# Optimization experiments

Measured on AMD Instinct MI355X. Metric: run time of the kernel, lower is better.

Reference implementation:

```python
import jax, jax.numpy as jnp
import numpy as np

THRESH = 0.5
IOU_THR = 0.3
TOP_K = 512

# standard YOLOv3 anchors for strides 32/16/8 (grids 13/26/52)
ANCHORS_13 = jnp.array([[116., 90.], [156., 198.], [373., 326.]], dtype=jnp.float32)
ANCHORS_26 = jnp.array([[30., 61.], [62., 45.], [59., 119.]], dtype=jnp.float32)
ANCHORS_52 = jnp.array([[10., 13.], [16., 30.], [33., 23.]], dtype=jnp.float32)


def _decode(out, stride, anchors):
    # out: [B, 3*(5+C), H, W] -> [B, H, W, 3, 5+C] (matches permute(0,2,3,1).reshape)
    B, _, H, W = out.shape
    o = jnp.transpose(out, (0, 2, 3, 1)).reshape(B, H, W, 3, -1)
    conf = jax.nn.sigmoid(o[..., 4])          # [B,H,W,3]
    xy = jax.nn.sigmoid(o[..., 0:2])          # sigmoid on x,y as in _filter
    gy = jnp.arange(H, dtype=o.dtype)[None, :, None, None]   # idxs[:,1]
    gx = jnp.arange(W, dtype=o.dtype)[None, None, :, None]   # idxs[:,2]
    cy = (gy + xy[..., 1]) * stride
    cx = (gx + xy[..., 0]) * stride
    w = anchors[:, 0] * jnp.exp(o[..., 2])    # anchors broadcast over anchor dim
    h = anchors[:, 1] * jnp.exp(o[..., 3])
    cls = jnp.argmax(o[..., 5:], axis=-1).astype(o.dtype)
    n = jnp.broadcast_to(jnp.arange(B, dtype=o.dtype)[:, None, None, None], conf.shape)
    w0, h0 = w * 0.5, h * 0.5
    boxes = jnp.stack([conf, cx - w0, cy - h0, cx + w0, cy + h0, cls, n], axis=-1)
    return boxes.reshape(-1, 7), conf.reshape(-1)


def _iou_matrix(b):
    # b: [K,4] = x1,y1,x2,y2 -> [K,K] IoU
    area = jnp.clip(b[:, 2] - b[:, 0], 0) * jnp.clip(b[:, 3] - b[:, 1], 0)
    xx1 = jnp.maximum(b[:, None, 0], b[None, :, 0])
    yy1 = jnp.maximum(b[:, None, 1], b[None, :, 1])
    xx2 = jnp.minimum(b[:, None, 2], b[None, :, 2])
    yy2 = jnp.minimum(b[:, None, 3], b[None, :, 3])
    inter = jnp.clip(xx2 - xx1, 0) * jnp.clip(yy2 - yy1, 0)
    return inter / (area[:, None] + area[None, :] - inter + 1e-9)


def _detect(output_13, output_26, output_52):
    b13, c13 = _decode(output_13, 32.0, ANCHORS_13)
    b26, c26 = _decode(output_26, 16.0, ANCHORS_26)
    b52, c52 = _decode(output_52, 8.0, ANCHORS_52)
    boxes = jnp.concatenate([b13, b26, b52], axis=0)      # [N,7]
    conf = jnp.concatenate([c13, c26, c52], axis=0)       # [N]
    # threshold filter (mask instead of nonzero-compaction for fixed shapes)
    scores = jnp.where(conf > THRESH, conf, 0.0)
    top_scores, idx = jax.lax.top_k(scores, TOP_K)        # sorted descending
    cand = boxes[idx]                                      # [K,7]
    valid = top_scores > THRESH
    iou = _iou_matrix(cand[:, 1:5])
    ar = jnp.arange(TOP_K)

    def body(i, keep):
        sup = keep[i] & (iou[i] > IOU_THR) & (ar > i)
        return keep & ~sup

    keep = jax.lax.fori_loop(0, TOP_K, body, valid)
    # zero out suppressed / invalid rows; rows: [conf, x1, y1, x2, y2, cls, batch]
    return cand * keep[:, None].astype(cand.dtype)


def setup_inputs() -> dict:
    key = jax.random.key(0)
    k1, k2, k3 = jax.random.split(key, 3)
    return {
        "output_13": jax.random.normal(k1, (32, 255, 13, 13), dtype=jnp.float32),
        "output_26": jax.random.normal(k2, (32, 255, 26, 26), dtype=jnp.float32),
        "output_52": jax.random.normal(k3, (32, 255, 52, 52), dtype=jnp.float32),
    }


def reference(output_13, output_26, output_52):
    return _detect(output_13, output_26, output_52)
```

## Files before the change

kernel.cpp:

```cpp
#include <hip/hip_runtime.h>

#define N13E 16224
#define N26E 64896
#define NTOT 340704
#define BASE26 16224
#define BASE52 81120
#define KMAX 2048
#define TOPK 512

__device__ __forceinline__ float sigm(float x) { return 1.0f / (1.0f + expf(-x)); }

__device__ __forceinline__ unsigned long long pack_key(float v, int c) {
    unsigned u = __float_as_uint(v);
    unsigned ov = (u & 0x80000000u) ? ~u : (u | 0x80000000u);
    return (((unsigned long long)ov) << 32) | (unsigned long long)(unsigned)(127 - c);
}

template <int HW>
__device__ __forceinline__ float load_logit(const float* __restrict__ p, int local) {
    int ba = local / HW;
    int hw = local - ba * HW;
    int b = ba / 3;
    int a = ba - b * 3;
    return p[(b * 255 + a * 85 + 4) * HW + hw];
}

__global__ void __launch_bounds__(256) k_hist(const float* __restrict__ p13,
                                              const float* __restrict__ p26,
                                              const float* __restrict__ p52,
                                              unsigned* __restrict__ hist) {
    int t = blockIdx.x * 256 + threadIdx.x;
    if (t >= NTOT) return;
    float logit;
    if (t < N13E)               logit = load_logit<169>(p13, t);
    else if (t < N13E + N26E)   logit = load_logit<676>(p26, t - N13E);
    else                        logit = load_logit<2704>(p52, t - (N13E + N26E));
    float conf = sigm(logit);
    if (conf > 0.5f) {
        unsigned bin = (__float_as_uint(conf) >> 12) - 0x3F000u;
        bin = (bin > 2047u) ? 2047u : bin;
        atomicAdd(&hist[bin], 1u);
    }
}

template <int HW, int BASE>
__device__ __forceinline__ void compact_one(const float* __restrict__ p, int local, unsigned thrv,
                                            unsigned* __restrict__ cnt,
                                            unsigned long long* __restrict__ keys) {
    int ba = local / HW;
    int hw = local - ba * HW;
    int b = ba / 3;
    int a = ba - b * 3;
    float logit = p[(b * 255 + a * 85 + 4) * HW + hw];
    float conf = sigm(logit);
    unsigned bits = __float_as_uint(conf);
    if (conf > 0.5f && bits >= thrv) {
        unsigned pos = atomicAdd(cnt, 1u);
        if (pos < (unsigned)KMAX) {
            unsigned concat = (unsigned)(BASE + (b * HW + hw) * 3 + a);
            keys[pos] = (((unsigned long long)bits) << 32) | (unsigned long long)(0xFFFFFFFFu - concat);
        }
    }
}

__global__ void __launch_bounds__(512) k_compact_scan(const float* __restrict__ p13,
                                                      const float* __restrict__ p26,
                                                      const float* __restrict__ p52,
                                                      const unsigned* __restrict__ hist,
                                                      unsigned* __restrict__ cnt,
                                                      unsigned long long* __restrict__ keys) {
    __shared__ unsigned tot[512];
    __shared__ unsigned thrS;
    int tid = threadIdx.x;

    unsigned loc[4]; unsigned s = 0u;
#pragma unroll
    for (int k = 0; k < 4; ++k) { loc[k] = hist[2047 - (tid * 4 + k)]; s += loc[k]; }
    tot[tid] = s;
    __syncthreads();
    for (int off = 1; off < 512; off <<= 1) {
        unsigned u = (tid >= off) ? tot[tid - off] : 0u;
        __syncthreads();
        tot[tid] += u;
        __syncthreads();
    }
    unsigned excl = tot[tid] - s;
    unsigned total = tot[511];
    if (total < (unsigned)TOPK) {
        if (tid == 0) thrS = 0x3F000001u;
    } else {
        unsigned run = excl;
#pragma unroll
        for (int k = 0; k < 4; ++k) {
            unsigned c = run + loc[k];
            if (run < (unsigned)TOPK && c >= (unsigned)TOPK) {
                int bin = 2047 - (tid * 4 + k);
                thrS = ((unsigned)(bin + 0x3F000)) << 12;
            }
            run = c;
        }
    }
    __syncthreads();
    unsigned thrv = thrS;

    int t = blockIdx.x * 512 + tid;
    if (t >= NTOT) return;
    if (t < N13E)               compact_one<169, 0>(p13, t, thrv, cnt, keys);
    else if (t < N13E + N26E)   compact_one<676, BASE26>(p26, t - N13E, thrv, cnt, keys);
    else                        compact_one<2704, BASE52>(p52, t - (N13E + N26E), thrv, cnt, keys);
}

template <int HW, int W>
__device__ __forceinline__ void decode64(const float* __restrict__ p, int local, float strideF,
                                         float aw0, float ah0, float aw1, float ah1, float aw2, float ah2,
                                         float conf, float* __restrict__ outrow, int lane) {
    int a = local % 3;
    int cell = local / 3;
    int b = cell / HW;
    int hw = cell - b * HW;
    int h = hw / W;
    int wc = hw - h * W;
    int cb = b * 255 + a * 85;
    float v1 = p[(cb + 5 + lane) * HW + hw];
    unsigned long long k1 = pack_key(v1, lane);
    if (lane < 16) {
        float v2 = p[(cb + 69 + lane) * HW + hw];
        unsigned long long k2 = pack_key(v2, lane + 64);
        if (k2 > k1) k1 = k2;
    }
#pragma unroll
    for (int m = 32; m >= 1; m >>= 1) {
        unsigned long long o = __shfl_xor(k1, m, 64);
        if (o > k1) k1 = o;
    }
    if (lane == 0) {
        int cls = 127 - (int)(unsigned)(k1 & 0xFFFFFFFFull);
        float t0 = p[(cb + 0) * HW + hw];
        float t1 = p[(cb + 1) * HW + hw];
        float t2 = p[(cb + 2) * HW + hw];
        float t3 = p[(cb + 3) * HW + hw];
        float aw = (a == 0) ? aw0 : ((a == 1) ? aw1 : aw2);
        float ah = (a == 0) ? ah0 : ((a == 1) ? ah1 : ah2);
        float sx = sigm(t0);
        float sy = sigm(t1);
        float bw = aw * expf(t2);
        float bh = ah * expf(t3);
        float cx = ((float)wc + sx) * strideF;
        float cy = ((float)h + sy) * strideF;
        float w0 = bw * 0.5f, h0 = bh * 0.5f;
        outrow[0] = conf;
        outrow[1] = cx - w0;
        outrow[2] = cy - h0;
        outrow[3] = cx + w0;
        outrow[4] = cy + h0;
        outrow[5] = (float)cls;
        outrow[6] = (float)b;
    }
}

__global__ void __launch_bounds__(512) k_rank_decode(const float* __restrict__ p13,
                                                     const float* __restrict__ p26,
                                                     const float* __restrict__ p52,
                                                     const unsigned* __restrict__ cnt,
                                                     const unsigned long long* __restrict__ keys,
                                                     float* __restrict__ cand) {
    __shared__ unsigned long long keysL[KMAX];
    __shared__ unsigned long long sortedL[8];
    int tid = threadIdx.x;

    unsigned n = *cnt; if (n > (unsigned)KMAX) n = (unsigned)KMAX;
    int npad = ((int)n + 7) & ~7;
    for (int j = tid; j < npad; j += 512) keysL[j] = (j < (int)n) ? keys[j] : 0ull;
    if (tid < 8) sortedL[tid] = 0ull;
    __syncthreads();
    int lo = blockIdx.x * 8;
    unsigned long long mine[4]; unsigned rk[4]; int nown = 0;
#pragma unroll
    for (int k = 0; k < 4; ++k) {
        int idx = tid + k * 512;
        if (idx < (int)n) { mine[nown] = keysL[idx]; rk[nown] = 0u; ++nown; }
    }
    for (int j = 0; j < npad; j += 8) {
        unsigned long long kk[8];
#pragma unroll
        for (int u = 0; u < 8; ++u) kk[u] = keysL[j + u];
        for (int m = 0; m < nown; ++m) {
            unsigned acc = 0u;
#pragma unroll
            for (int u = 0; u < 8; ++u) acc += (kk[u] > mine[m]) ? 1u : 0u;
            rk[m] += acc;
        }
    }
    for (int m = 0; m < nown; ++m) {
        unsigned r = rk[m];
        if (r >= (unsigned)lo && r < (unsigned)(lo + 8)) sortedL[r - lo] = mine[m];
    }
    __syncthreads();

    int bb = tid >> 6;
    int lane = tid & 63;
    int box = lo + bb;
    unsigned long long key = sortedL[bb];
    unsigned sb = (unsigned)(key >> 32);
    float* row = cand + box * 7;
    if (sb == 0u) {
        if (lane < 7) row[lane] = 0.0f;
        return;
    }
    unsigned idx = 0xFFFFFFFFu - (unsigned)(key & 0xFFFFFFFFull);
    float conf = __uint_as_float(sb);
    if (idx < N13E)
        decode64<169, 13>(p13, (int)idx, 32.0f, 116.f, 90.f, 156.f, 198.f, 373.f, 326.f, conf, row, lane);
    else if (idx < N13E + N26E)
        decode64<676, 26>(p26, (int)idx - BASE26, 16.0f, 30.f, 61.f, 62.f, 45.f, 59.f, 119.f, conf, row, lane);
    else
        decode64<2704, 52>(p52, (int)idx - BASE52, 8.0f, 10.f, 13.f, 16.f, 30.f, 33.f, 23.f, conf, row, lane);
}

__global__ void __launch_bounds__(512) k_mask(const float* __restrict__ cand,
                                              unsigned long long* __restrict__ smaskG) {
    __shared__ float sx1[TOPK], sy1[TOPK], sx2[TOPK], sy2[TOPK];
    int tid = threadIdx.x;
    for (int p = tid; p < TOPK; p += 512) {
        const float* r = cand + p * 7;
        sx1[p] = r[1]; sy1[p] = r[2]; sx2[p] = r[3]; sy2[p] = r[4];
    }
    __syncthreads();
    int wv = tid >> 6;
    int lane = tid & 63;
    int gwave = blockIdx.x * 8 + wv;
#pragma unroll
    for (int q = 0; q < 16; ++q) {
        int word = gwave * 16 + q;
        int i = word >> 3, jw = word & 7;
        int j = jw * 64 + lane;
        float ix1 = sx1[i], iy1 = sy1[i], ix2 = sx2[i], iy2 = sy2[i];
        float ai = fmaxf(ix2 - ix1, 0.f) * fmaxf(iy2 - iy1, 0.f);
        float jx1 = sx1[j], jy1 = sy1[j], jx2 = sx2[j], jy2 = sy2[j];
        float aj = fmaxf(jx2 - jx1, 0.f) * fmaxf(jy2 - jy1, 0.f);
        float xx1 = fmaxf(ix1, jx1), yy1 = fmaxf(iy1, jy1);
        float xx2 = fminf(ix2, jx2), yy2 = fminf(iy2, jy2);
        float inter = fmaxf(xx2 - xx1, 0.f) * fmaxf(yy2 - yy1, 0.f);
        float iou = inter / (((ai + aj) - inter) + 1e-9f);
        bool bit = (j > i) && (iou > 0.3f);
        unsigned long long m = __ballot(bit);
        if (lane == 0) smaskG[word] = m;
    }
}

__global__ void __launch_bounds__(512) k_sweep(const float* __restrict__ cand,
                                               const unsigned long long* __restrict__ smaskG,
                                               float* __restrict__ out) {
    __shared__ unsigned long long smask[TOPK * 8];
    __shared__ unsigned long long live[8], keepw[8];
    int tid = threadIdx.x;
    for (int p = tid; p < TOPK * 8; p += 512) smask[p] = smaskG[p];
    bool validt = cand[tid * 7] > 0.5f;
    unsigned long long bal = __ballot(validt);
    if ((tid & 63) == 0) live[tid >> 6] = bal;
    __syncthreads();
    if (tid < 64) {
        int lane = tid;
        int lw = lane & 7;
        unsigned long long r = 0ull;
#pragma unroll
        for (int w = 0; w < 8; ++w) {
            unsigned long long lvw = live[w];
#pragma unroll 8
            for (int b2 = 0; b2 < 64; ++b2) {
                int i = w * 64 + b2;
                unsigned long long rowv = smask[i * 8 + lw];
                unsigned rlo = (unsigned)__builtin_amdgcn_readlane((int)(unsigned)(r & 0xFFFFFFFFull), w);
                unsigned rhi = (unsigned)__builtin_amdgcn_readlane((int)(unsigned)(r >> 32), w);
                unsigned long long rw = (((unsigned long long)rhi) << 32) | (unsigned long long)rlo;
                bool acc = (((lvw >> b2) & 1ull) != 0ull) && (((rw >> b2) & 1ull) == 0ull);
                if (acc) r |= rowv;
            }
        }
        if (lane < 8) keepw[lane] = live[lane] & ~r;
    }
    __syncthreads();
    for (int p = tid; p < TOPK * 7; p += 512) {
        int i = p / 7;
        unsigned long long kb = (keepw[i >> 6] >> (i & 63)) & 1ull;
        out[p] = kb ? cand[p] : 0.0f;
    }
}

extern "C" void kernel_launch(void* const* d_in, const int* in_sizes, int n_in,
                              void* d_out, int out_size, void* d_ws, size_t ws_size,
                              hipStream_t stream) {
    const float* p13 = (const float*)d_in[0];
    const float* p26 = (const float*)d_in[1];
    const float* p52 = (const float*)d_in[2];
    float* out = (float*)d_out;
    char* ws = (char*)d_ws;

    unsigned* hist             = (unsigned*)(ws + 0);
    unsigned* cnt              = (unsigned*)(ws + 8192);
    unsigned long long* keys   = (unsigned long long*)(ws + 8704);
    float* cand                = (float*)(ws + 25088);
    unsigned long long* smaskG = (unsigned long long*)(ws + 39936);

    hipMemsetAsync(ws, 0, 8196, stream);

    int gh = (NTOT + 255) / 256;
    int gc = (NTOT + 511) / 512;
    k_hist<<<gh, 256, 0, stream>>>(p13, p26, p52, hist);
    k_compact_scan<<<gc, 512, 0, stream>>>(p13, p26, p52, hist, cnt, keys);
    k_rank_decode<<<64, 512, 0, stream>>>(p13, p26, p52, cnt, keys, cand);
    k_mask<<<32, 512, 0, stream>>>(cand, smaskG);
    k_sweep<<<1, 512, 0, stream>>>(cand, smaskG, out);
}
```

Baseline: 234.4 us.

## Fuse all detection stages into one cooperative persistent kernel with grid syncs

Replaces the memset and five separate launches (histogram, threshold scan plus compaction, rank/decode, IoU mask, sweep) with a single cooperative kernel of 256 blocks that separates phases with grid.sync. Each thread keeps its confidence values in registers across phases, so the logits are no longer read twice. The goal is to remove launch overhead and inter-kernel gaps. In exchange it adds several grid-wide barriers, redoes the threshold scan in every block, leaves most blocks idle during the serial sweep, and depends on all 256 blocks being co-resident.

```diff
diff --git a/kernel.cpp b/kernel.cpp
--- a/kernel.cpp
+++ b/kernel.cpp
@@ -1,4 +1,7 @@
 #include <hip/hip_runtime.h>
+#include <hip/hip_cooperative_groups.h>
+
+namespace cg = cooperative_groups;
 
 #define N13E 16224
 #define N26E 64896
@@ -7,6 +10,9 @@
 #define BASE52 81120
 #define KMAX 2048
 #define TOPK 512
+#define GRID 256
+#define BLOCK 512
+#define GTHREADS (GRID * BLOCK)
 
 __device__ __forceinline__ float sigm(float x) { return 1.0f / (1.0f + expf(-x)); }
 
@@ -16,98 +22,20 @@
     return (((unsigned long long)ov) << 32) | (unsigned long long)(unsigned)(127 - c);
 }
 
-template <int HW>
-__device__ __forceinline__ float load_logit(const float* __restrict__ p, int local) {
-    int ba = local / HW;
-    int hw = local - ba * HW;
-    int b = ba / 3;
-    int a = ba - b * 3;
-    return p[(b * 255 + a * 85 + 4) * HW + hw];
-}
-
-__global__ void __launch_bounds__(256) k_hist(const float* __restrict__ p13,
-                                              const float* __restrict__ p26,
-                                              const float* __restrict__ p52,
-                                              unsigned* __restrict__ hist) {
-    int t = blockIdx.x * 256 + threadIdx.x;
-    if (t >= NTOT) return;
-    float logit;
-    if (t < N13E)               logit = load_logit<169>(p13, t);
-    else if (t < N13E + N26E)   logit = load_logit<676>(p26, t - N13E);
-    else                        logit = load_logit<2704>(p52, t - (N13E + N26E));
-    float conf = sigm(logit);
-    if (conf > 0.5f) {
-        unsigned bin = (__float_as_uint(conf) >> 12) - 0x3F000u;
-        bin = (bin > 2047u) ? 2047u : bin;
-        atomicAdd(&hist[bin], 1u);
-    }
-}
-
 template <int HW, int BASE>
-__device__ __forceinline__ void compact_one(const float* __restrict__ p, int local, unsigned thrv,
-                                            unsigned* __restrict__ cnt,
-                                            unsigned long long* __restrict__ keys) {
+__device__ __forceinline__ void conf_one(const float* __restrict__ p, int local,
+                                         unsigned& bits, unsigned& concat, bool& pass) {
     int ba = local / HW;
     int hw = local - ba * HW;
     int b = ba / 3;
     int a = ba - b * 3;
     float logit = p[(b * 255 + a * 85 + 4) * HW + hw];
     float conf = sigm(logit);
-    unsigned bits = __float_as_uint(conf);
-    if (conf > 0.5f && bits >= thrv) {
-        unsigned pos = atomicAdd(cnt, 1u);
-        if (pos < (unsigned)KMAX) {
-            unsigned concat = (unsigned)(BASE + (b * HW + hw) * 3 + a);
-            keys[pos] = (((unsigned long long)bits) << 32) | (unsigned long long)(0xFFFFFFFFu - concat);
-        }
-    }
-}
-
-__global__ void __launch_bounds__(512) k_compact_scan(const float* __restrict__ p13,
-                                                      const float* __restrict__ p26,
-                                                      const float* __restrict__ p52,
-                                                      const unsigned* __restrict__ hist,
-                                                      unsigned* __restrict__ cnt,
-                                                      unsigned long long* __restrict__ keys) {
-    __shared__ unsigned tot[512];
-    __shared__ unsigned thrS;
-    int tid = threadIdx.x;
-
-    unsigned loc[4]; unsigned s = 0u;
-#pragma unroll
-    for (int k = 0; k < 4; ++k) { loc[k] = hist[2047 - (tid * 4 + k)]; s += loc[k]; }
-    tot[tid] = s;
-    __syncthreads();
-    for (int off = 1; off < 512; off <<= 1) {
-        unsigned u = (tid >= off) ? tot[tid - off] : 0u;
-        __syncthreads();
-        tot[tid] += u;
-        __syncthreads();
-    }
-    unsigned excl = tot[tid] - s;
-    unsigned total = tot[511];
-    if (total < (unsigned)TOPK) {
-        if (tid == 0) thrS = 0x3F000001u;
-    } else {
-        unsigned run = excl;
-#pragma unroll
-        for (int k = 0; k < 4; ++k) {
-            unsigned c = run + loc[k];
-            if (run < (unsigned)TOPK && c >= (unsigned)TOPK) {
-                int bin = 2047 - (tid * 4 + k);
-                thrS = ((unsigned)(bin + 0x3F000)) << 12;
-            }
-            run = c;
-        }
-    }
-    __syncthreads();
-    unsigned thrv = thrS;
-
-    int t = blockIdx.x * 512 + tid;
-    if (t >= NTOT) return;
-    if (t < N13E)               compact_one<169, 0>(p13, t, thrv, cnt, keys);
-    else if (t < N13E + N26E)   compact_one<676, BASE26>(p26, t - N13E, thrv, cnt, keys);
-    else                        compact_one<2704, BASE52>(p52, t - (N13E + N26E), thrv, cnt, keys);
+    if (conf > 0.5f) {
+        pass = true;
+        bits = __float_as_uint(conf);
+        concat = (unsigned)(BASE + (b * HW + hw) * 3 + a);
+    }
 }
 
 template <int HW, int W>
@@ -158,132 +86,216 @@
     }
 }
 
-__global__ void __launch_bounds__(512) k_rank_decode(const float* __restrict__ p13,
-                                                     const float* __restrict__ p26,
-                                                     const float* __restrict__ p52,
-                                                     const unsigned* __restrict__ cnt,
-                                                     const unsigned long long* __restrict__ keys,
-                                                     float* __restrict__ cand) {
-    __shared__ unsigned long long keysL[KMAX];
-    __shared__ unsigned long long sortedL[8];
+union SharedU {
+    struct { unsigned tot[BLOCK]; unsigned thrS; } scan;
+    struct { unsigned long long keysL[KMAX]; unsigned long long sortedL[2]; } rank;
+    struct { float sx1[TOPK]; float sy1[TOPK]; float sx2[TOPK]; float sy2[TOPK]; } mask;
+    struct { unsigned long long smask[TOPK * 8]; unsigned long long live[8];
+             unsigned long long keepw[8]; } sweep;
+};
+
+__global__ void __launch_bounds__(BLOCK, 2) k_fused(
+    const float* __restrict__ p13, const float* __restrict__ p26, const float* __restrict__ p52,
+    unsigned* __restrict__ hist, unsigned* __restrict__ cnt,
+    unsigned long long* __restrict__ keys, float* __restrict__ cand,
+    unsigned long long* __restrict__ smaskG, float* __restrict__ out) {
+
+    cg::grid_group grid = cg::this_grid();
+    __shared__ SharedU sh;
     int tid = threadIdx.x;
-
-    unsigned n = *cnt; if (n > (unsigned)KMAX) n = (unsigned)KMAX;
-    int npad = ((int)n + 7) & ~7;
-    for (int j = tid; j < npad; j += 512) keysL[j] = (j < (int)n) ? keys[j] : 0ull;
-    if (tid < 8) sortedL[tid] = 0ull;
-    __syncthreads();
-    int lo = blockIdx.x * 8;
-    unsigned long long mine[4]; unsigned rk[4]; int nown = 0;
-#pragma unroll
-    for (int k = 0; k < 4; ++k) {
-        int idx = tid + k * 512;
-        if (idx < (int)n) { mine[nown] = keysL[idx]; rk[nown] = 0u; ++nown; }
-    }
-    for (int j = 0; j < npad; j += 8) {
-        unsigned long long kk[8];
-#pragma unroll
-        for (int u = 0; u < 8; ++u) kk[u] = keysL[j + u];
+    int gid = blockIdx.x * BLOCK + tid;
+
+    if (gid < 2048) hist[gid] = 0u;
+    if (gid == 2048) *cnt = 0u;
+
+    unsigned bits0 = 0, bits1 = 0, bits2 = 0;
+    unsigned conc0 = 0, conc1 = 0, conc2 = 0;
+    bool pass0 = false, pass1 = false, pass2 = false;
+    {
+        int e = gid;
+        if (e < N13E)             conf_one<169, 0>(p13, e, bits0, conc0, pass0);
+        else if (e < N13E + N26E) conf_one<676, BASE26>(p26, e - N13E, bits0, conc0, pass0);
+        else                      conf_one<2704, BASE52>(p52, e - (N13E + N26E), bits0, conc0, pass0);
+    }
+    {
+        int e = gid + GTHREADS;
+        conf_one<2704, BASE52>(p52, e - (N13E + N26E), bits1, conc1, pass1);
+    }
+    {
+        int e = gid + 2 * GTHREADS;
+        if (e < NTOT) conf_one<2704, BASE52>(p52, e - (N13E + N26E), bits2, conc2, pass2);
+    }
+    grid.sync();
+
+    {
+        if (pass0) { unsigned bin = (bits0 >> 12) - 0x3F000u; bin = (bin > 2047u) ? 2047u : bin; atomicAdd(&hist[bin], 1u); }
+        if (pass1) { unsigned bin = (bits1 >> 12) - 0x3F000u; bin = (bin > 2047u) ? 2047u : bin; atomicAdd(&hist[bin], 1u); }
+        if (pass2) { unsigned bin = (bits2 >> 12) - 0x3F000u; bin = (bin > 2047u) ? 2047u : bin; atomicAdd(&hist[bin], 1u); }
+    }
+    grid.sync();
+
+    {
+        unsigned loc[4]; unsigned s = 0u;
+#pragma unroll
+        for (int k = 0; k < 4; ++k) { loc[k] = hist[2047 - (tid * 4 + k)]; s += loc[k]; }
+        sh.scan.tot[tid] = s;
+        __syncthreads();
+        for (int off = 1; off < BLOCK; off <<= 1) {
+            unsigned u = (tid >= off) ? sh.scan.tot[tid - off] : 0u;
+            __syncthreads();
+            sh.scan.tot[tid] += u;
+            __syncthreads();
+        }
+        unsigned excl = sh.scan.tot[tid] - s;
+        unsigned total = sh.scan.tot[BLOCK - 1];
+        if (total < (unsigned)TOPK) {
+            if (tid == 0) sh.scan.thrS = 0x3F000001u;
+        } else {
+            unsigned run = excl;
+#pragma unroll
+            for (int k = 0; k < 4; ++k) {
+                unsigned c = run + loc[k];
+                if (run < (unsigned)TOPK && c >= (unsigned)TOPK) {
+                    int bin = 2047 - (tid * 4 + k);
+                    sh.scan.thrS = ((unsigned)(bin + 0x3F000)) << 12;
+                }
+                run = c;
+            }
+        }
+        __syncthreads();
+        unsigned thrv = sh.scan.thrS;
+        if (pass0 && bits0 >= thrv) {
+            unsigned pos = atomicAdd(cnt, 1u);
+            if (pos < (unsigned)KMAX)
+                keys[pos] = (((unsigned long long)bits0) << 32) | (unsigned long long)(0xFFFFFFFFu - conc0);
+        }
+        if (pass1 && bits1 >= thrv) {
+            unsigned pos = atomicAdd(cnt, 1u);
+            if (pos < (unsigned)KMAX)
+                keys[pos] = (((unsigned long long)bits1) << 32) | (unsigned long long)(0xFFFFFFFFu - conc1);
+        }
+        if (pass2 && bits2 >= thrv) {
+            unsigned pos = atomicAdd(cnt, 1u);
+            if (pos < (unsigned)KMAX)
+                keys[pos] = (((unsigned long long)bits2) << 32) | (unsigned long long)(0xFFFFFFFFu - conc2);
+        }
+    }
+    grid.sync();
+
+    {
+        unsigned n = *cnt; if (n > (unsigned)KMAX) n = (unsigned)KMAX;
+        int npad = ((int)n + 7) & ~7;
+        for (int j = tid; j < npad; j += BLOCK) sh.rank.keysL[j] = (j < (int)n) ? keys[j] : 0ull;
+        if (tid < 2) sh.rank.sortedL[tid] = 0ull;
+        __syncthreads();
+        int lo = blockIdx.x * 2;
+        unsigned long long mine[4]; unsigned rk[4]; int nown = 0;
+#pragma unroll
+        for (int k = 0; k < 4; ++k) {
+            int idx = tid + k * BLOCK;
+            if (idx < (int)n) { mine[nown] = sh.rank.keysL[idx]; rk[nown] = 0u; ++nown; }
+        }
+        for (int j = 0; j < npad; j += 8) {
+            unsigned long long kk[8];
+#pragma unroll
+            for (int u = 0; u < 8; ++u) kk[u] = sh.rank.keysL[j + u];
+            for (int m = 0; m < nown; ++m) {
+                unsigned acc = 0u;
+#pragma unroll
+                for (int u = 0; u < 8; ++u) acc += (kk[u] > mine[m]) ? 1u : 0u;
+                rk[m] += acc;
+            }
+        }
         for (int m = 0; m < nown; ++m) {
-            unsigned acc = 0u;
-#pragma unroll
-            for (int u = 0; u < 8; ++u) acc += (kk[u] > mine[m]) ? 1u : 0u;
-            rk[m] += acc;
-        }
-    }
-    for (int m = 0; m < nown; ++m) {
-        unsigned r = rk[m];
-        if (r >= (unsigned)lo && r < (unsigned)(lo + 8)) sortedL[r - lo] = mine[m];
-    }
-    __syncthreads();
-
-    int bb = tid >> 6;
-    int lane = tid & 63;
-    int box = lo + bb;
-    unsigned long long key = sortedL[bb];
-    unsigned sb = (unsigned)(key >> 32);
-    float* row = cand + box * 7;
-    if (sb == 0u) {
-        if (lane < 7) row[lane] = 0.0f;
-        return;
-    }
-    unsigned idx = 0xFFFFFFFFu - (unsigned)(key & 0xFFFFFFFFull);
-    float conf = __uint_as_float(sb);
-    if (idx < N13E)
-        decode64<169, 13>(p13, (int)idx, 32.0f, 116.f, 90.f, 156.f, 198.f, 373.f, 326.f, conf, row, lane);
-    else if (idx < N13E + N26E)
-        decode64<676, 26>(p26, (int)idx - BASE26, 16.0f, 30.f, 61.f, 62.f, 45.f, 59.f, 119.f, conf, row, lane);
-    else
-        decode64<2704, 52>(p52, (int)idx - BASE52, 8.0f, 10.f, 13.f, 16.f, 30.f, 33.f, 23.f, conf, row, lane);
-}
-
-__global__ void __launch_bounds__(512) k_mask(const float* __restrict__ cand,
-                                              unsigned long long* __restrict__ smaskG) {
-    __shared__ float sx1[TOPK], sy1[TOPK], sx2[TOPK], sy2[TOPK];
-    int tid = threadIdx.x;
-    for (int p = tid; p < TOPK; p += 512) {
-        const float* r = cand + p * 7;
-        sx1[p] = r[1]; sy1[p] = r[2]; sx2[p] = r[3]; sy2[p] = r[4];
-    }
-    __syncthreads();
-    int wv = tid >> 6;
-    int lane = tid & 63;
-    int gwave = blockIdx.x * 8 + wv;
-#pragma unroll
-    for (int q = 0; q < 16; ++q) {
-        int word = gwave * 16 + q;
-        int i = word >> 3, jw = word & 7;
-        int j = jw * 64 + lane;
-        float ix1 = sx1[i], iy1 = sy1[i], ix2 = sx2[i], iy2 = sy2[i];
-        float ai = fmaxf(ix2 - ix1, 0.f) * fmaxf(iy2 - iy1, 0.f);
-        float jx1 = sx1[j], jy1 = sy1[j], jx2 = sx2[j], jy2 = sy2[j];
-        float aj = fmaxf(jx2 - jx1, 0.f) * fmaxf(jy2 - jy1, 0.f);
-        float xx1 = fmaxf(ix1, jx1), yy1 = fmaxf(iy1, jy1);
-        float xx2 = fminf(ix2, jx2), yy2 = fminf(iy2, jy2);
-        float inter = fmaxf(xx2 - xx1, 0.f) * fmaxf(yy2 - yy1, 0.f);
-        float iou = inter / (((ai + aj) - inter) + 1e-9f);
-        bool bit = (j > i) && (iou > 0.3f);
-        unsigned long long m = __ballot(bit);
-        if (lane == 0) smaskG[word] = m;
-    }
-}
-
-__global__ void __launch_bounds__(512) k_sweep(const float* __restrict__ cand,
-                                               const unsigned long long* __restrict__ smaskG,
-                                               float* __restrict__ out) {
-    __shared__ unsigned long long smask[TOPK * 8];
-    __shared__ unsigned long long live[8], keepw[8];
-    int tid = threadIdx.x;
-    for (int p = tid; p < TOPK * 8; p += 512) smask[p] = smaskG[p];
-    bool validt = cand[tid * 7] > 0.5f;
-    unsigned long long bal = __ballot(validt);
-    if ((tid & 63) == 0) live[tid >> 6] = bal;
-    __syncthreads();
-    if (tid < 64) {
-        int lane = tid;
-        int lw = lane & 7;
-        unsigned long long r = 0ull;
-#pragma unroll
-        for (int w = 0; w < 8; ++w) {
-            unsigned long long lvw = live[w];
+            unsigned r = rk[m];
+            if (r >= (unsigned)lo && r < (unsigned)(lo + 2)) sh.rank.sortedL[r - lo] = mine[m];
+        }
+        __syncthreads();
+
+        int bb = tid >> 6;
+        int lane = tid & 63;
+        if (bb < 2) {
+            int box = lo + bb;
+            unsigned long long key = sh.rank.sortedL[bb];
+            unsigned sb = (unsigned)(key >> 32);
+            float* row = cand + box * 7;
+            if (sb == 0u) {
+                if (lane < 7) row[lane] = 0.0f;
+            } else {
+                unsigned idx = 0xFFFFFFFFu - (unsigned)(key & 0xFFFFFFFFull);
+                float conf = __uint_as_float(sb);
+                if (idx < N13E)
+                    decode64<169, 13>(p13, (int)idx, 32.0f, 116.f, 90.f, 156.f, 198.f, 373.f, 326.f, conf, row, lane);
+                else if (idx < N13E + N26E)
+                    decode64<676, 26>(p26, (int)idx - BASE26, 16.0f, 30.f, 61.f, 62.f, 45.f, 59.f, 119.f, conf, row, lane);
+                else
+                    decode64<2704, 52>(p52, (int)idx - BASE52, 8.0f, 10.f, 13.f, 16.f, 30.f, 33.f, 23.f, conf, row, lane);
+            }
+        }
+    }
+    grid.sync();
+
+    {
+        for (int p = tid; p < TOPK; p += BLOCK) {
+            const float* r = cand + p * 7;
+            sh.mask.sx1[p] = r[1]; sh.mask.sy1[p] = r[2]; sh.mask.sx2[p] = r[3]; sh.mask.sy2[p] = r[4];
+        }
+        __syncthreads();
+        int wv = tid >> 6;
+        int lane = tid & 63;
+        int gwave = blockIdx.x * 8 + wv;
+#pragma unroll
+        for (int q = 0; q < 2; ++q) {
+            int word = gwave * 2 + q;
+            int i = word >> 3, jw = word & 7;
+            int j = jw * 64 + lane;
+            float ix1 = sh.mask.sx1[i], iy1 = sh.mask.sy1[i], ix2 = sh.mask.sx2[i], iy2 = sh.mask.sy2[i];
+            float ai = fmaxf(ix2 - ix1, 0.f) * fmaxf(iy2 - iy1, 0.f);
+            float jx1 = sh.mask.sx1[j], jy1 = sh.mask.sy1[j], jx2 = sh.mask.sx2[j], jy2 = sh.mask.sy2[j];
+            float aj = fmaxf(jx2 - jx1, 0.f) * fmaxf(jy2 - jy1, 0.f);
+            float xx1 = fmaxf(ix1, jx1), yy1 = fmaxf(iy1, jy1);
+            float xx2 = fminf(ix2, jx2), yy2 = fminf(iy2, jy2);
+            float inter = fmaxf(xx2 - xx1, 0.f) * fmaxf(yy2 - yy1, 0.f);
+            float iou = inter / (((ai + aj) - inter) + 1e-9f);
+            bool bit = (j > i) && (iou > 0.3f);
+            unsigned long long m = __ballot(bit);
+            if (lane == 0) smaskG[word] = m;
+        }
+    }
+    grid.sync();
+
+    if (blockIdx.x == 0) {
+        for (int p = tid; p < TOPK * 8; p += BLOCK) sh.sweep.smask[p] = smaskG[p];
+        bool validt = cand[tid * 7] > 0.5f;
+        unsigned long long bal = __ballot(validt);
+        if ((tid & 63) == 0) sh.sweep.live[tid >> 6] = bal;
+        __syncthreads();
+        if (tid < 64) {
+            int lane = tid;
+            int lw = lane & 7;
+            unsigned long long r = 0ull;
+#pragma unroll
+            for (int w = 0; w < 8; ++w) {
+                unsigned long long lvw = sh.sweep.live[w];
 #pragma unroll 8
-            for (int b2 = 0; b2 < 64; ++b2) {
-                int i = w * 64 + b2;
-                unsigned long long rowv = smask[i * 8 + lw];
-                unsigned rlo = (unsigned)__builtin_amdgcn_readlane((int)(unsigned)(r & 0xFFFFFFFFull), w);
-                unsigned rhi = (unsigned)__builtin_amdgcn_readlane((int)(unsigned)(r >> 32), w);
-                unsigned long long rw = (((unsigned long long)rhi) << 32) | (unsigned long long)rlo;
-                bool acc = (((lvw >> b2) & 1ull) != 0ull) && (((rw >> b2) & 1ull) == 0ull);
-                if (acc) r |= rowv;
+                for (int b2 = 0; b2 < 64; ++b2) {
+                    int i = w * 64 + b2;
+                    unsigned long long rowv = sh.sweep.smask[i * 8 + lw];
+                    unsigned rlo = (unsigned)__builtin_amdgcn_readlane((int)(unsigned)(r & 0xFFFFFFFFull), w);
+                    unsigned rhi = (unsigned)__builtin_amdgcn_readlane((int)(unsigned)(r >> 32), w);
+                    unsigned long long rw = (((unsigned long long)rhi) << 32) | (unsigned long long)rlo;
+                    bool acc = (((lvw >> b2) & 1ull) != 0ull) && (((rw >> b2) & 1ull) == 0ull);
+                    if (acc) r |= rowv;
+                }
             }
-        }
-        if (lane < 8) keepw[lane] = live[lane] & ~r;
-    }
-    __syncthreads();
-    for (int p = tid; p < TOPK * 7; p += 512) {
-        int i = p / 7;
-        unsigned long long kb = (keepw[i >> 6] >> (i & 63)) & 1ull;
-        out[p] = kb ? cand[p] : 0.0f;
+            if (lane < 8) sh.sweep.keepw[lane] = sh.sweep.live[lane] & ~r;
+        }
+        __syncthreads();
+        for (int p = tid; p < TOPK * 7; p += BLOCK) {
+            int i = p / 7;
+            unsigned long long kb = (sh.sweep.keepw[i >> 6] >> (i & 63)) & 1ull;
+            out[p] = kb ? cand[p] : 0.0f;
+        }
     }
 }
 
@@ -302,13 +314,9 @@
     float* cand                = (float*)(ws + 25088);
     unsigned long long* smaskG = (unsigned long long*)(ws + 39936);
 
-    hipMemsetAsync(ws, 0, 8196, stream);
-
-    int gh = (NTOT + 255) / 256;
-    int gc = (NTOT + 511) / 512;
-    k_hist<<<gh, 256, 0, stream>>>(p13, p26, p52, hist);
-    k_compact_scan<<<gc, 512, 0, stream>>>(p13, p26, p52, hist, cnt, keys);
-    k_rank_decode<<<64, 512, 0, stream>>>(p13, p26, p52, cnt, keys, cand);
-    k_mask<<<32, 512, 0, stream>>>(cand, smaskG);
-    k_sweep<<<1, 512, 0, stream>>>(cand, smaskG, out);
-}
+    void* args[] = { (void*)&p13, (void*)&p26, (void*)&p52,
+                     (void*)&hist, (void*)&cnt, (void*)&keys,
+                     (void*)&cand, (void*)&smaskG, (void*)&out };
+    hipLaunchCooperativeKernel((const void*)k_fused, dim3(GRID), dim3(BLOCK),
+                               args, 0, stream);
+}
```

Result: slower. 363.6 us (+55.1%).

## Fuse rank, decode, IoU mask and sweep into one single-block kernel

Applied to the files above, without the earlier changes.

Replaces the three tail kernels (rank+decode over 64 blocks, mask over 32 blocks, sweep on 1 block) with one 512-thread block that ranks, decodes, builds the IoU suppression mask in shared memory and runs the sweep. Each thread now decodes one box and does a serial 80-way argmax instead of spreading it across a wavefront with shuffles, and mask words entirely below the diagonal are skipped. This removes two kernel launches and the global round trips for candidates and mask, at the cost of running all ranking and mask work on a single CU and a longer serial argmax per thread.

```diff
diff --git a/kernel.cpp b/kernel.cpp
--- a/kernel.cpp
+++ b/kernel.cpp
@@ -9,12 +9,6 @@
 #define TOPK 512
 
 __device__ __forceinline__ float sigm(float x) { return 1.0f / (1.0f + expf(-x)); }
-
-__device__ __forceinline__ unsigned long long pack_key(float v, int c) {
-    unsigned u = __float_as_uint(v);
-    unsigned ov = (u & 0x80000000u) ? ~u : (u | 0x80000000u);
-    return (((unsigned long long)ov) << 32) | (unsigned long long)(unsigned)(127 - c);
-}
 
 template <int HW>
 __device__ __forceinline__ float load_logit(const float* __restrict__ p, int local) {
@@ -111,9 +105,9 @@
 }
 
 template <int HW, int W>
-__device__ __forceinline__ void decode64(const float* __restrict__ p, int local, float strideF,
-                                         float aw0, float ah0, float aw1, float ah1, float aw2, float ah2,
-                                         float conf, float* __restrict__ outrow, int lane) {
+__device__ __forceinline__ void decode1(const float* __restrict__ p, int local, float strideF,
+                                        float aw0, float ah0, float aw1, float ah1, float aw2, float ah2,
+                                        float conf, float* __restrict__ row) {
     int a = local % 3;
     int cell = local / 3;
     int b = cell / HW;
@@ -121,59 +115,54 @@
     int h = hw / W;
     int wc = hw - h * W;
     int cb = b * 255 + a * 85;
-    float v1 = p[(cb + 5 + lane) * HW + hw];
-    unsigned long long k1 = pack_key(v1, lane);
-    if (lane < 16) {
-        float v2 = p[(cb + 69 + lane) * HW + hw];
-        unsigned long long k2 = pack_key(v2, lane + 64);
-        if (k2 > k1) k1 = k2;
-    }
-#pragma unroll
-    for (int m = 32; m >= 1; m >>= 1) {
-        unsigned long long o = __shfl_xor(k1, m, 64);
-        if (o > k1) k1 = o;
-    }
-    if (lane == 0) {
-        int cls = 127 - (int)(unsigned)(k1 & 0xFFFFFFFFull);
-        float t0 = p[(cb + 0) * HW + hw];
-        float t1 = p[(cb + 1) * HW + hw];
-        float t2 = p[(cb + 2) * HW + hw];
-        float t3 = p[(cb + 3) * HW + hw];
-        float aw = (a == 0) ? aw0 : ((a == 1) ? aw1 : aw2);
-        float ah = (a == 0) ? ah0 : ((a == 1) ? ah1 : ah2);
-        float sx = sigm(t0);
-        float sy = sigm(t1);
-        float bw = aw * expf(t2);
-        float bh = ah * expf(t3);
-        float cx = ((float)wc + sx) * strideF;
-        float cy = ((float)h + sy) * strideF;
-        float w0 = bw * 0.5f, h0 = bh * 0.5f;
-        outrow[0] = conf;
-        outrow[1] = cx - w0;
-        outrow[2] = cy - h0;
-        outrow[3] = cx + w0;
-        outrow[4] = cy + h0;
-        outrow[5] = (float)cls;
-        outrow[6] = (float)b;
-    }
-}
-
-__global__ void __launch_bounds__(512) k_rank_decode(const float* __restrict__ p13,
-                                                     const float* __restrict__ p26,
-                                                     const float* __restrict__ p52,
-                                                     const unsigned* __restrict__ cnt,
-                                                     const unsigned long long* __restrict__ keys,
-                                                     float* __restrict__ cand) {
+    const float* cls_base = p + (size_t)(cb + 5) * HW + hw;
+    float bestv = cls_base[0];
+    int bestc = 0;
+#pragma unroll
+    for (int c = 1; c < 80; ++c) {
+        float v = cls_base[(size_t)c * HW];
+        if (v > bestv) { bestv = v; bestc = c; }
+    }
+    float t0 = p[(size_t)(cb + 0) * HW + hw];
+    float t1 = p[(size_t)(cb + 1) * HW + hw];
+    float t2 = p[(size_t)(cb + 2) * HW + hw];
+    float t3 = p[(size_t)(cb + 3) * HW + hw];
+    float aw = (a == 0) ? aw0 : ((a == 1) ? aw1 : aw2);
+    float ah = (a == 0) ? ah0 : ((a == 1) ? ah1 : ah2);
+    float sx = sigm(t0);
+    float sy = sigm(t1);
+    float bw = aw * expf(t2);
+    float bh = ah * expf(t3);
+    float cx = ((float)wc + sx) * strideF;
+    float cy = ((float)h + sy) * strideF;
+    float w0 = bw * 0.5f, h0 = bh * 0.5f;
+    row[0] = conf;
+    row[1] = cx - w0;
+    row[2] = cy - h0;
+    row[3] = cx + w0;
+    row[4] = cy + h0;
+    row[5] = (float)bestc;
+    row[6] = (float)b;
+}
+
+__global__ void __launch_bounds__(512) k_mega(const float* __restrict__ p13,
+                                              const float* __restrict__ p26,
+                                              const float* __restrict__ p52,
+                                              const unsigned* __restrict__ cnt,
+                                              const unsigned long long* __restrict__ keys,
+                                              float* __restrict__ out) {
     __shared__ unsigned long long keysL[KMAX];
-    __shared__ unsigned long long sortedL[8];
+    __shared__ unsigned long long sortedL[TOPK];
+    __shared__ float candL[TOPK * 7];
+    __shared__ unsigned long long smask[TOPK * 8];
+    __shared__ unsigned long long live[8], keepw[8];
     int tid = threadIdx.x;
 
     unsigned n = *cnt; if (n > (unsigned)KMAX) n = (unsigned)KMAX;
     int npad = ((int)n + 7) & ~7;
     for (int j = tid; j < npad; j += 512) keysL[j] = (j < (int)n) ? keys[j] : 0ull;
-    if (tid < 8) sortedL[tid] = 0ull;
-    __syncthreads();
-    int lo = blockIdx.x * 8;
+    sortedL[tid] = 0ull;
+    __syncthreads();
     unsigned long long mine[4]; unsigned rk[4]; int nown = 0;
 #pragma unroll
     for (int k = 0; k < 4; ++k) {
@@ -193,69 +182,56 @@
     }
     for (int m = 0; m < nown; ++m) {
         unsigned r = rk[m];
-        if (r >= (unsigned)lo && r < (unsigned)(lo + 8)) sortedL[r - lo] = mine[m];
-    }
-    __syncthreads();
-
-    int bb = tid >> 6;
-    int lane = tid & 63;
-    int box = lo + bb;
-    unsigned long long key = sortedL[bb];
-    unsigned sb = (unsigned)(key >> 32);
-    float* row = cand + box * 7;
-    if (sb == 0u) {
-        if (lane < 7) row[lane] = 0.0f;
-        return;
-    }
-    unsigned idx = 0xFFFFFFFFu - (unsigned)(key & 0xFFFFFFFFull);
-    float conf = __uint_as_float(sb);
-    if (idx < N13E)
-        decode64<169, 13>(p13, (int)idx, 32.0f, 116.f, 90.f, 156.f, 198.f, 373.f, 326.f, conf, row, lane);
-    else if (idx < N13E + N26E)
-        decode64<676, 26>(p26, (int)idx - BASE26, 16.0f, 30.f, 61.f, 62.f, 45.f, 59.f, 119.f, conf, row, lane);
-    else
-        decode64<2704, 52>(p52, (int)idx - BASE52, 8.0f, 10.f, 13.f, 16.f, 30.f, 33.f, 23.f, conf, row, lane);
-}
-
-__global__ void __launch_bounds__(512) k_mask(const float* __restrict__ cand,
-                                              unsigned long long* __restrict__ smaskG) {
-    __shared__ float sx1[TOPK], sy1[TOPK], sx2[TOPK], sy2[TOPK];
-    int tid = threadIdx.x;
-    for (int p = tid; p < TOPK; p += 512) {
-        const float* r = cand + p * 7;
-        sx1[p] = r[1]; sy1[p] = r[2]; sx2[p] = r[3]; sy2[p] = r[4];
-    }
-    __syncthreads();
-    int wv = tid >> 6;
-    int lane = tid & 63;
-    int gwave = blockIdx.x * 8 + wv;
-#pragma unroll
-    for (int q = 0; q < 16; ++q) {
-        int word = gwave * 16 + q;
-        int i = word >> 3, jw = word & 7;
-        int j = jw * 64 + lane;
-        float ix1 = sx1[i], iy1 = sy1[i], ix2 = sx2[i], iy2 = sy2[i];
-        float ai = fmaxf(ix2 - ix1, 0.f) * fmaxf(iy2 - iy1, 0.f);
-        float jx1 = sx1[j], jy1 = sy1[j], jx2 = sx2[j], jy2 = sy2[j];
-        float aj = fmaxf(jx2 - jx1, 0.f) * fmaxf(jy2 - jy1, 0.f);
-        float xx1 = fmaxf(ix1, jx1), yy1 = fmaxf(iy1, jy1);
-        float xx2 = fminf(ix2, jx2), yy2 = fminf(iy2, jy2);
-        float inter = fmaxf(xx2 - xx1, 0.f) * fmaxf(yy2 - yy1, 0.f);
-        float iou = inter / (((ai + aj) - inter) + 1e-9f);
-        bool bit = (j > i) && (iou > 0.3f);
-        unsigned long long m = __ballot(bit);
-        if (lane == 0) smaskG[word] = m;
-    }
-}
-
-__global__ void __launch_bounds__(512) k_sweep(const float* __restrict__ cand,
-                                               const unsigned long long* __restrict__ smaskG,
-                                               float* __restrict__ out) {
-    __shared__ unsigned long long smask[TOPK * 8];
-    __shared__ unsigned long long live[8], keepw[8];
-    int tid = threadIdx.x;
-    for (int p = tid; p < TOPK * 8; p += 512) smask[p] = smaskG[p];
-    bool validt = cand[tid * 7] > 0.5f;
+        if (r < (unsigned)TOPK) sortedL[r] = mine[m];
+    }
+    __syncthreads();
+
+    {
+        unsigned long long key = sortedL[tid];
+        unsigned sb = (unsigned)(key >> 32);
+        float* row = candL + tid * 7;
+        if (sb == 0u) {
+#pragma unroll
+            for (int q = 0; q < 7; ++q) row[q] = 0.0f;
+        } else {
+            unsigned idx = 0xFFFFFFFFu - (unsigned)(key & 0xFFFFFFFFull);
+            float conf = __uint_as_float(sb);
+            if (idx < N13E)
+                decode1<169, 13>(p13, (int)idx, 32.0f, 116.f, 90.f, 156.f, 198.f, 373.f, 326.f, conf, row);
+            else if (idx < N13E + N26E)
+                decode1<676, 26>(p26, (int)idx - BASE26, 16.0f, 30.f, 61.f, 62.f, 45.f, 59.f, 119.f, conf, row);
+            else
+                decode1<2704, 52>(p52, (int)idx - BASE52, 8.0f, 10.f, 13.f, 16.f, 30.f, 33.f, 23.f, conf, row);
+        }
+    }
+    __syncthreads();
+
+    {
+        int wv = tid >> 6;
+        int lane = tid & 63;
+        for (int word = wv; word < TOPK * 8; word += 8) {
+            int i = word >> 3, jw = word & 7;
+            if ((jw << 6) + 63 <= i) {
+                if (lane == 0) smask[word] = 0ull;
+                continue;
+            }
+            int j = (jw << 6) + lane;
+            const float* ri = candL + i * 7;
+            const float* rj = candL + j * 7;
+            float ix1 = ri[1], iy1 = ri[2], ix2 = ri[3], iy2 = ri[4];
+            float ai = fmaxf(ix2 - ix1, 0.f) * fmaxf(iy2 - iy1, 0.f);
+            float jx1 = rj[1], jy1 = rj[2], jx2 = rj[3], jy2 = rj[4];
+            float aj = fmaxf(jx2 - jx1, 0.f) * fmaxf(jy2 - jy1, 0.f);
+            float xx1 = fmaxf(ix1, jx1), yy1 = fmaxf(iy1, jy1);
+            float xx2 = fminf(ix2, jx2), yy2 = fminf(iy2, jy2);
+            float inter = fmaxf(xx2 - xx1, 0.f) * fmaxf(yy2 - yy1, 0.f);
+            float iou = inter / (((ai + aj) - inter) + 1e-9f);
+            bool bit = (j > i) && (iou > 0.3f);
+            unsigned long long m = __ballot(bit);
+            if (lane == 0) smask[word] = m;
+        }
+    }
+    bool validt = candL[tid * 7] > 0.5f;
     unsigned long long bal = __ballot(validt);
     if ((tid & 63) == 0) live[tid >> 6] = bal;
     __syncthreads();
@@ -283,7 +259,7 @@
     for (int p = tid; p < TOPK * 7; p += 512) {
         int i = p / 7;
         unsigned long long kb = (keepw[i >> 6] >> (i & 63)) & 1ull;
-        out[p] = kb ? cand[p] : 0.0f;
+        out[p] = kb ? candL[p] : 0.0f;
     }
 }
 
@@ -296,11 +272,9 @@
     float* out = (float*)d_out;
     char* ws = (char*)d_ws;
 
-    unsigned* hist             = (unsigned*)(ws + 0);
-    unsigned* cnt              = (unsigned*)(ws + 8192);
-    unsigned long long* keys   = (unsigned long long*)(ws + 8704);
-    float* cand                = (float*)(ws + 25088);
-    unsigned long long* smaskG = (unsigned long long*)(ws + 39936);
+    unsigned* hist           = (unsigned*)(ws + 0);
+    unsigned* cnt            = (unsigned*)(ws + 8192);
+    unsigned long long* keys = (unsigned long long*)(ws + 8704);
 
     hipMemsetAsync(ws, 0, 8196, stream);
 
@@ -308,7 +282,5 @@
     int gc = (NTOT + 511) / 512;
     k_hist<<<gh, 256, 0, stream>>>(p13, p26, p52, hist);
     k_compact_scan<<<gc, 512, 0, stream>>>(p13, p26, p52, hist, cnt, keys);
-    k_rank_decode<<<64, 512, 0, stream>>>(p13, p26, p52, cnt, keys, cand);
-    k_mask<<<32, 512, 0, stream>>>(cand, smaskG);
-    k_sweep<<<1, 512, 0, stream>>>(cand, smaskG, out);
-}
+    k_mega<<<1, 512, 0, stream>>>(p13, p26, p52, cnt, keys, out);
+}
```

New measurement: 446.9 us. 90.7% more time.
